# Kernel optimization log

Hardware: AMD Instinct MI355X
Metric: run time of the kernel (lower is better)

The kernel has to match this reference:

```python
import jax, jax.numpy as jnp
import numpy as np

N = 50000      # query points
N0 = 50000     # support points
M = 32         # neighbors per query
K = 15         # kernel points
DIM = 3
D_IN = 64
D_OUT = 64
POINT_INFLUENCE = 1.0
KERNEL_RADIUS = 1.5 * POINT_INFLUENCE  # _INFLUENCE_TO_RADIUS * point_influence


def setup_inputs() -> dict:
    key = jax.random.key(0)
    k1, k2, k3, k4, k5 = jax.random.split(key, 5)
    query_points = jax.random.normal(k1, (N, DIM), jnp.float32)
    support_points = jax.random.normal(k2, (N0, DIM), jnp.float32)
    neighbors = jax.random.randint(k3, (N, M), 0, N0 + 1)  # index N0 = shadow point
    x = jax.random.normal(k4, (N0, D_IN), jnp.float32)
    # Kernel point dispositions: fixed center point, rest spread within kernel radius
    # (stand-in for kernel_point_optimization_debug; K_points is a frozen parameter).
    rng = np.random.RandomState(0)
    kp = rng.uniform(-1.0, 1.0, (K, DIM))
    kp[0, :] = 0.0
    kp = kp * (KERNEL_RADIUS / np.max(np.linalg.norm(kp, axis=1)))
    K_points = jnp.asarray(kp, dtype=jnp.float32)
    # Xavier-normal conv weights [K, D_IN, D_OUT]
    std = (2.0 / (D_IN + D_OUT)) ** 0.5
    weight = jax.random.normal(k5, (K, D_IN, D_OUT), jnp.float32) * std
    return {
        "query_points": query_points,
        "support_points": support_points,
        "neighbors": neighbors,
        "x": x,
        "K_points": K_points,
        "weight": weight,
    }


def reference(query_points, support_points, neighbors, x, K_points, weight):
    # Shadow support point far away + zero shadow feature row
    shadow = jnp.full((1, query_points.shape[1]), 1e6, dtype=support_points.dtype)
    sp = jnp.concatenate([support_points, shadow], axis=0)            # [N0+1, 3]
    xp = jnp.concatenate([x, jnp.zeros((1, x.shape[1]), x.dtype)], axis=0)  # [N0+1, d]

    # Gather neighbor coords, center on query point
    neighb_pts = sp[neighbors] - query_points[:, None, :]             # [N, M, 3]
    # Squared distances to each kernel point
    diff = neighb_pts[:, :, None, :] - K_points[None, None, :, :]     # [N, M, K, 3]
    sq_distances = jnp.sum(diff * diff, axis=-1)                      # [N, M, K]

    # Linear influence, then transpose to [N, K, M]
    all_weights = jnp.clip(1.0 - jnp.sqrt(sq_distances) / POINT_INFLUENCE, 0.0)
    all_weights = jnp.swapaxes(all_weights, 1, 2)                     # [N, K, M]

    # Gather neighbor features and aggregate per kernel point
    feats = xp[neighbors]                                             # [N, M, d]
    weighted = jnp.einsum("nkm,nmd->nkd", all_weights, feats)        # [N, K, d]
    # Apply per-kernel-point weight matrices and sum over kernel points
    out = jnp.einsum("nkd,kdo->no", weighted, weight)                # [N, out]
    return out
```

## Files before the change

### kernel.cpp

```cpp
#include <hip/hip_runtime.h>

#define NQ 50000
#define NS 50000
#define MNB 32
#define KP 15
#define DF 64
#define WTS 968
#define WQS 40

typedef __bf16 bf16x8 __attribute__((ext_vector_type(8)));
typedef float  f32x4  __attribute__((ext_vector_type(4)));

__device__ __forceinline__ unsigned short bf1(float f) {
    union { __bf16 h; unsigned short s; } r; r.h = (__bf16)f; return r.s;
}
__device__ __forceinline__ unsigned pk2(float a, float b) {
    union { __bf16 h[2]; unsigned u; } r;
    r.h[0] = (__bf16)a; r.h[1] = (__bf16)b; return r.u;
}

__global__ __launch_bounds__(256) void preconv(
    const float* __restrict__ x, const float* __restrict__ W,
    unsigned short* __restrict__ xbp, uint4* __restrict__ wBf)
{
    const int b = blockIdx.x;
    if (b < NS / 16) {
        const int row = b * 16 + (threadIdx.x >> 4);
        const int cl  = threadIdx.x & 15;
        const float f0 = x[row * DF + 0 * 16 + cl];
        const float f1 = x[row * DF + 1 * 16 + cl];
        const float f2 = x[row * DF + 2 * 16 + cl];
        const float f3 = x[row * DF + 3 * 16 + cl];
        uint2 o; o.x = pk2(f0, f1); o.y = pk2(f2, f3);
        *(uint2*)&xbp[row * DF + cl * 4] = o;
    } else if (b < NS / 16 + 30) {
        const int chunk = (b - NS / 16) * 256 + threadIdx.x;
        const int tc = chunk >> 6, c = chunk & 63;
        union { unsigned short s[8]; uint4 u; } pk;
        #pragma unroll
        for (int j = 0; j < 8; ++j) {
            const int kappa = tc * 8 + j;
            const int k  = kappa >> 6;
            const int cb = kappa & 3;
            const int t  = (kappa >> 2) & 15;
            pk.s[j] = bf1(W[(size_t)(k * 64 + cb * 16 + t) * 64 + c]);
        }
        wBf[chunk] = pk.u;
    } else {
        if (threadIdx.x < 8)
            ((uint4*)(xbp + (size_t)NS * DF))[threadIdx.x] = (uint4){0, 0, 0, 0};
    }
}

__global__ __launch_bounds__(1024, 8) void kpconv_fused(
    const float* __restrict__ qp, const float* __restrict__ sp,
    const int* __restrict__ nb, const uint2* __restrict__ xb2,
    const float* __restrict__ kpts, const uint4* __restrict__ wBf,
    float* __restrict__ out)
{
    __shared__ struct {
        __align__(16) unsigned short wt[16 * WTS];
        __align__(16) unsigned short wq[16][16 * WQS];
        __align__(16) unsigned int   ids[16][MNB];
    } sm;

    const int tid  = threadIdx.x;
    const int lane = tid & 63, wv = tid >> 6;
    const int kh = lane >> 5, m = lane & 31;
    const int n0 = blockIdx.x * 16;
    const int n  = n0 + wv;

    const int id = nb[n * MNB + m];
    const float qx = qp[n * 3 + 0], qy = qp[n * 3 + 1], qz = qp[n * 3 + 2];
    float sx = 1e6f, sy = 1e6f, sz = 1e6f;
    if (id < NS) { sx = sp[id * 3 + 0]; sy = sp[id * 3 + 1]; sz = sp[id * 3 + 2]; }
    const float rx = sx - qx, ry = sy - qy, rz = sz - qz;
    float wk[8], wmax = 0.0f;
    #pragma unroll
    for (int j = 0; j < 8; ++j) {
        const int k = kh * 8 + j;
        const int kc = (k < KP) ? k : 0;
        const float dx = rx - kpts[kc * 3 + 0];
        const float dy = ry - kpts[kc * 3 + 1];
        const float dz = rz - kpts[kc * 3 + 2];
        wk[j] = fmaxf(1.0f - sqrtf(dx * dx + dy * dy + dz * dz), 0.0f);
        wmax = fmaxf(wmax, wk[j]);
    }
    const unsigned long long bal = __ballot(wmax > 0.0f);
    const unsigned comb = (unsigned)(bal & 0xFFFFFFFFull) | (unsigned)(bal >> 32);
    const int A = __popc(comb);
    const bool act = (comb >> m) & 1u;
    const unsigned mlow = (1u << m) - 1u;
    const int p = act ? __popc(comb & mlow) : (A + __popc(~comb & mlow));
    const int s = (p & 3) * 8 + (p >> 2);
    #pragma unroll
    for (int j = 0; j < 8; ++j) {
        const int k = kh * 8 + j;
        if (k < KP) sm.wq[wv][k * WQS + s] = bf1(wk[j]);
    }
    if (kh == 0) sm.ids[wv][p] = act ? (unsigned)id : (unsigned)NS;

    const int cl = lane & 15, q = lane >> 4;
    union { uint4 u; bf16x8 v; } af;
    af.u = *(const uint4*)&sm.wq[wv][cl * WQS + q * 8];
    uint2 r[8];
    #pragma unroll
    for (int j = 0; j < 8; ++j) r[j] = (uint2){0u, 0u};
    #pragma unroll
    for (int j = 0; j < 8; ++j) {
        if (4 * j < A) {
            const unsigned sid = sm.ids[wv][4 * j + q];
            r[j] = xb2[(size_t)sid * 16 + cl];
        }
    }
    #define PRM(hi, lo, sel) __builtin_amdgcn_perm((hi), (lo), (sel))
    const unsigned S0 = 0x05040100u, S1 = 0x07060302u;
    union { uint4 u; bf16x8 v; } bf[4];
    bf[0].u = (uint4){PRM(r[1].x, r[0].x, S0), PRM(r[3].x, r[2].x, S0), PRM(r[5].x, r[4].x, S0), PRM(r[7].x, r[6].x, S0)};
    bf[1].u = (uint4){PRM(r[1].x, r[0].x, S1), PRM(r[3].x, r[2].x, S1), PRM(r[5].x, r[4].x, S1), PRM(r[7].x, r[6].x, S1)};
    bf[2].u = (uint4){PRM(r[1].y, r[0].y, S0), PRM(r[3].y, r[2].y, S0), PRM(r[5].y, r[4].y, S0), PRM(r[7].y, r[6].y, S0)};
    bf[3].u = (uint4){PRM(r[1].y, r[0].y, S1), PRM(r[3].y, r[2].y, S1), PRM(r[5].y, r[4].y, S1), PRM(r[7].y, r[6].y, S1)};
    #undef PRM
    const f32x4 zero = (f32x4){0.f, 0.f, 0.f, 0.f};
    f32x4 acc1[4];
    #pragma unroll
    for (int cb = 0; cb < 4; ++cb)
        acc1[cb] = __builtin_amdgcn_mfma_f32_16x16x32_bf16(af.v, bf[cb].v, zero, 0, 0, 0);

    #pragma unroll
    for (int i = 0; i < 4; ++i) {
        const int k = q * 4 + i;
        if (k < KP) {
            uint2 pkd;
            pkd.x = pk2(acc1[0][i], acc1[1][i]);
            pkd.y = pk2(acc1[2][i], acc1[3][i]);
            *(uint2*)&sm.wt[wv * WTS + (k * 16 + cl) * 4] = pkd;
        }
    }
    __syncthreads();
    if (wv >= 4) return;

    f32x4 dacc = (f32x4){0.f, 0.f, 0.f, 0.f};
    #pragma unroll 6
    for (int ks = 0; ks < 30; ++ks) {
        const bf16x8 a = *(const bf16x8*)&sm.wt[cl * WTS + ks * 32 + q * 8];
        union { uint4 u; bf16x8 v; } bu;
        bu.u = wBf[(4 * ks + q) * 64 + wv * 16 + cl];
        dacc = __builtin_amdgcn_mfma_f32_16x16x32_bf16(a, bu.v, dacc, 0, 0, 0);
    }
    #pragma unroll
    for (int i = 0; i < 4; ++i)
        out[(size_t)(n0 + q * 4 + i) * 64 + wv * 16 + cl] = dacc[i];
}

extern "C" void kernel_launch(void* const* d_in, const int* in_sizes, int n_in,
                              void* d_out, int out_size, void* d_ws, size_t ws_size,
                              hipStream_t stream) {
    const float* qp   = (const float*)d_in[0];
    const float* sp   = (const float*)d_in[1];
    const int*   nb   = (const int*)d_in[2];
    const float* x    = (const float*)d_in[3];
    const float* kpts = (const float*)d_in[4];
    const float* W    = (const float*)d_in[5];
    float* out = (float*)d_out;

    uint4*          wBf = (uint4*)d_ws;
    unsigned short* xbp = (unsigned short*)((char*)d_ws + 122880);

    hipLaunchKernelGGL(preconv, dim3(NS / 16 + 31), dim3(256), 0, stream,
                       x, W, xbp, wBf);
    hipLaunchKernelGGL(kpconv_fused, dim3(NQ / 16), dim3(1024), 0, stream,
                       qp, sp, nb, (const uint2*)xbp, kpts, wBf, out);
}
```

Before: 126.5 us.

## Gather fp32 features directly and drop the bf16 pre-conversion pass over x

Removes the pass that converted the whole feature matrix x to bf16 before the main kernel. The fused kernel now gathers fp32 float4 rows straight from x and packs them to bf16 in registers, so only the small weight conversion kernel remains. This saves a full read and write of x and the extra work in the launch, but each gather now reads twice as many bytes. Smaller tweaks are also included: distance math done in pairs with a hardware sqrt, a scalar wave index, and weights gated in place of branching.

```diff
diff --git a/kernel.cpp b/kernel.cpp
--- a/kernel.cpp
+++ b/kernel.cpp
@@ -10,6 +10,7 @@
 
 typedef __bf16 bf16x8 __attribute__((ext_vector_type(8)));
 typedef float  f32x4  __attribute__((ext_vector_type(4)));
+typedef float  f32x2  __attribute__((ext_vector_type(2)));
 
 __device__ __forceinline__ unsigned short bf1(float f) {
     union { __bf16 h; unsigned short s; } r; r.h = (__bf16)f; return r.s;
@@ -19,42 +20,20 @@
     r.h[0] = (__bf16)a; r.h[1] = (__bf16)b; return r.u;
 }
 
-__global__ __launch_bounds__(256) void preconv(
-    const float* __restrict__ x, const float* __restrict__ W,
-    unsigned short* __restrict__ xbp, uint4* __restrict__ wBf)
-{
-    const int b = blockIdx.x;
-    if (b < NS / 16) {
-        const int row = b * 16 + (threadIdx.x >> 4);
-        const int cl  = threadIdx.x & 15;
-        const float f0 = x[row * DF + 0 * 16 + cl];
-        const float f1 = x[row * DF + 1 * 16 + cl];
-        const float f2 = x[row * DF + 2 * 16 + cl];
-        const float f3 = x[row * DF + 3 * 16 + cl];
-        uint2 o; o.x = pk2(f0, f1); o.y = pk2(f2, f3);
-        *(uint2*)&xbp[row * DF + cl * 4] = o;
-    } else if (b < NS / 16 + 30) {
-        const int chunk = (b - NS / 16) * 256 + threadIdx.x;
-        const int tc = chunk >> 6, c = chunk & 63;
-        union { unsigned short s[8]; uint4 u; } pk;
-        #pragma unroll
-        for (int j = 0; j < 8; ++j) {
-            const int kappa = tc * 8 + j;
-            const int k  = kappa >> 6;
-            const int cb = kappa & 3;
-            const int t  = (kappa >> 2) & 15;
-            pk.s[j] = bf1(W[(size_t)(k * 64 + cb * 16 + t) * 64 + c]);
-        }
-        wBf[chunk] = pk.u;
-    } else {
-        if (threadIdx.x < 8)
-            ((uint4*)(xbp + (size_t)NS * DF))[threadIdx.x] = (uint4){0, 0, 0, 0};
-    }
+__global__ __launch_bounds__(256) void conv_w(const float* __restrict__ W,
+                                              uint4* __restrict__ wBf) {
+    const int chunk = blockIdx.x * 256 + threadIdx.x;
+    const int tc = chunk >> 6, c = chunk & 63;
+    union { unsigned short s[8]; uint4 u; } pk;
+    #pragma unroll
+    for (int j = 0; j < 8; ++j)
+        pk.s[j] = bf1(W[(size_t)(tc * 8 + j) * 64 + c]);
+    wBf[chunk] = pk.u;
 }
 
 __global__ __launch_bounds__(1024, 8) void kpconv_fused(
     const float* __restrict__ qp, const float* __restrict__ sp,
-    const int* __restrict__ nb, const uint2* __restrict__ xb2,
+    const int* __restrict__ nb, const float* __restrict__ x,
     const float* __restrict__ kpts, const uint4* __restrict__ wBf,
     float* __restrict__ out)
 {
@@ -65,7 +44,8 @@
     } sm;
 
     const int tid  = threadIdx.x;
-    const int lane = tid & 63, wv = tid >> 6;
+    const int lane = tid & 63;
+    const int wv   = __builtin_amdgcn_readfirstlane(tid >> 6);
     const int kh = lane >> 5, m = lane & 31;
     const int n0 = blockIdx.x * 16;
     const int n  = n0 + wv;
@@ -77,14 +57,18 @@
     const float rx = sx - qx, ry = sy - qy, rz = sz - qz;
     float wk[8], wmax = 0.0f;
     #pragma unroll
-    for (int j = 0; j < 8; ++j) {
-        const int k = kh * 8 + j;
-        const int kc = (k < KP) ? k : 0;
-        const float dx = rx - kpts[kc * 3 + 0];
-        const float dy = ry - kpts[kc * 3 + 1];
-        const float dz = rz - kpts[kc * 3 + 2];
-        wk[j] = fmaxf(1.0f - sqrtf(dx * dx + dy * dy + dz * dz), 0.0f);
-        wmax = fmaxf(wmax, wk[j]);
+    for (int jj = 0; jj < 4; ++jj) {
+        const int ka = kh * 8 + jj;
+        const int kb0 = ka + 4;
+        const int kb = (kb0 < KP) ? kb0 : 0;
+        const f32x2 dx = (f32x2){rx, rx} - (f32x2){kpts[ka*3+0], kpts[kb*3+0]};
+        const f32x2 dy = (f32x2){ry, ry} - (f32x2){kpts[ka*3+1], kpts[kb*3+1]};
+        const f32x2 dz = (f32x2){rz, rz} - (f32x2){kpts[ka*3+2], kpts[kb*3+2]};
+        const f32x2 d2 = dx * dx + dy * dy + dz * dz;
+        const float wa = fmaxf(1.0f - __builtin_amdgcn_sqrtf(d2.x), 0.0f);
+        const float wb = fmaxf(1.0f - __builtin_amdgcn_sqrtf(d2.y), 0.0f);
+        wk[jj] = wa; wk[jj + 4] = wb;
+        wmax = fmaxf(wmax, fmaxf(wa, wb));
     }
     const unsigned long long bal = __ballot(wmax > 0.0f);
     const unsigned comb = (unsigned)(bal & 0xFFFFFFFFull) | (unsigned)(bal >> 32);
@@ -93,39 +77,50 @@
     const unsigned mlow = (1u << m) - 1u;
     const int p = act ? __popc(comb & mlow) : (A + __popc(~comb & mlow));
     const int s = (p & 3) * 8 + (p >> 2);
+    const float gate = act ? 1.0f : 0.0f;
     #pragma unroll
-    for (int j = 0; j < 8; ++j) {
-        const int k = kh * 8 + j;
-        if (k < KP) sm.wq[wv][k * WQS + s] = bf1(wk[j]);
-    }
-    if (kh == 0) sm.ids[wv][p] = act ? (unsigned)id : (unsigned)NS;
+    for (int jj = 0; jj < 8; ++jj)
+        sm.wq[wv][(kh * 8 + jj) * WQS + s] = bf1(wk[jj] * gate);
+    if (kh == 0) sm.ids[wv][p] = act ? (unsigned)id : 0u;
 
     const int cl = lane & 15, q = lane >> 4;
     union { uint4 u; bf16x8 v; } af;
     af.u = *(const uint4*)&sm.wq[wv][cl * WQS + q * 8];
-    uint2 r[8];
-    #pragma unroll
-    for (int j = 0; j < 8; ++j) r[j] = (uint2){0u, 0u};
-    #pragma unroll
-    for (int j = 0; j < 8; ++j) {
-        if (4 * j < A) {
-            const unsigned sid = sm.ids[wv][4 * j + q];
-            r[j] = xb2[(size_t)sid * 16 + cl];
+    const float4* __restrict__ x4 = (const float4*)x;
+    union { uint4 u; bf16x8 v; } bfr[4];
+    {
+        float4 r[4];
+        #pragma unroll
+        for (int j = 0; j < 4; ++j) {
+            r[j] = (float4){0.f, 0.f, 0.f, 0.f};
+            if (4 * j < A)
+                r[j] = x4[(size_t)sm.ids[wv][4 * j + q] * 16 + cl];
+        }
+        #pragma unroll
+        for (int cb = 0; cb < 4; ++cb) {
+            bfr[cb].u.x = pk2(((const float*)&r[0])[cb], ((const float*)&r[1])[cb]);
+            bfr[cb].u.y = pk2(((const float*)&r[2])[cb], ((const float*)&r[3])[cb]);
         }
     }
-    #define PRM(hi, lo, sel) __builtin_amdgcn_perm((hi), (lo), (sel))
-    const unsigned S0 = 0x05040100u, S1 = 0x07060302u;
-    union { uint4 u; bf16x8 v; } bf[4];
-    bf[0].u = (uint4){PRM(r[1].x, r[0].x, S0), PRM(r[3].x, r[2].x, S0), PRM(r[5].x, r[4].x, S0), PRM(r[7].x, r[6].x, S0)};
-    bf[1].u = (uint4){PRM(r[1].x, r[0].x, S1), PRM(r[3].x, r[2].x, S1), PRM(r[5].x, r[4].x, S1), PRM(r[7].x, r[6].x, S1)};
-    bf[2].u = (uint4){PRM(r[1].y, r[0].y, S0), PRM(r[3].y, r[2].y, S0), PRM(r[5].y, r[4].y, S0), PRM(r[7].y, r[6].y, S0)};
-    bf[3].u = (uint4){PRM(r[1].y, r[0].y, S1), PRM(r[3].y, r[2].y, S1), PRM(r[5].y, r[4].y, S1), PRM(r[7].y, r[6].y, S1)};
-    #undef PRM
+    {
+        float4 r[4];
+        #pragma unroll
+        for (int j = 0; j < 4; ++j) {
+            r[j] = (float4){0.f, 0.f, 0.f, 0.f};
+            if (4 * (j + 4) < A)
+                r[j] = x4[(size_t)sm.ids[wv][4 * (j + 4) + q] * 16 + cl];
+        }
+        #pragma unroll
+        for (int cb = 0; cb < 4; ++cb) {
+            bfr[cb].u.z = pk2(((const float*)&r[0])[cb], ((const float*)&r[1])[cb]);
+            bfr[cb].u.w = pk2(((const float*)&r[2])[cb], ((const float*)&r[3])[cb]);
+        }
+    }
     const f32x4 zero = (f32x4){0.f, 0.f, 0.f, 0.f};
     f32x4 acc1[4];
     #pragma unroll
     for (int cb = 0; cb < 4; ++cb)
-        acc1[cb] = __builtin_amdgcn_mfma_f32_16x16x32_bf16(af.v, bf[cb].v, zero, 0, 0, 0);
+        acc1[cb] = __builtin_amdgcn_mfma_f32_16x16x32_bf16(af.v, bfr[cb].v, zero, 0, 0, 0);
 
     #pragma unroll
     for (int i = 0; i < 4; ++i) {
@@ -134,7 +129,7 @@
             uint2 pkd;
             pkd.x = pk2(acc1[0][i], acc1[1][i]);
             pkd.y = pk2(acc1[2][i], acc1[3][i]);
-            *(uint2*)&sm.wt[wv * WTS + (k * 16 + cl) * 4] = pkd;
+            *(uint2*)&sm.wt[wv * WTS + k * 64 + cl * 4] = pkd;
         }
     }
     __syncthreads();
@@ -164,11 +159,9 @@
     const float* W    = (const float*)d_in[5];
     float* out = (float*)d_out;
 
-    uint4*          wBf = (uint4*)d_ws;
-    unsigned short* xbp = (unsigned short*)((char*)d_ws + 122880);
+    uint4* wBf = (uint4*)d_ws;
 
-    hipLaunchKernelGGL(preconv, dim3(NS / 16 + 31), dim3(256), 0, stream,
-                       x, W, xbp, wBf);
+    hipLaunchKernelGGL(conv_w, dim3(30), dim3(256), 0, stream, W, wBf);
     hipLaunchKernelGGL(kpconv_fused, dim3(NQ / 16), dim3(1024), 0, stream,
-                       qp, sp, nb, (const uint2*)xbp, kpts, wBf, out);
+                       qp, sp, nb, x, kpts, wBf, out);
 }
```

Result: no change. 124.5 us (-1.5%).
